# Performance work log

Hardware: AMD Instinct MI355X
Metric: run time of the kernel (lower is better)

The kernel has to match this reference:

```python
import jax, jax.numpy as jnp
import numpy as np

N_HITS = 16384
N_EDGES = 262144
N_GROUPS = 512
N_EVENTS = 64
IN_CH = 25
HID = 128
HEADS = 4
DH = HID // HEADS
LAYERS = 3
EDGE_DIM = 5
FFN = 4 * HID
EPS = 1e-5


def setup_inputs() -> dict:
    key = jax.random.key(0)
    ks = jax.random.split(key, 16)
    def nrm(k, shape, s=0.05):
        return jax.random.normal(k, shape, dtype=jnp.float32) * s
    z = lambda *s: jnp.zeros(s, jnp.float32)
    return {
        "x": jax.random.normal(ks[0], (N_HITS, IN_CH), dtype=jnp.float32),
        "edge_index": jax.random.randint(ks[1], (2, N_EDGES), 0, N_HITS, dtype=jnp.int32),
        "edge_attr": jax.random.normal(ks[2], (N_EDGES, EDGE_DIM), dtype=jnp.float32),
        "group_indices": jax.random.randint(ks[3], (N_HITS,), 0, N_GROUPS, dtype=jnp.int32),
        "batch_indices_per_group": jnp.sort(jax.random.randint(ks[4], (N_GROUPS,), 0, N_EVENTS, dtype=jnp.int32)),
        "embed_W": nrm(ks[5], (IN_CH, HID)),
        "embed_b": z(HID),
        "blk_Wqkv": nrm(ks[6], (LAYERS, HID, 3 * HID)),
        "blk_bqkv": z(LAYERS, 3 * HID),
        "blk_We": nrm(ks[7], (LAYERS, EDGE_DIM, HID)),
        "blk_be": z(LAYERS, HID),
        "blk_Wo": nrm(ks[8], (LAYERS, HID, HID)),
        "blk_bo": z(LAYERS, HID),
        "ln1_g": jnp.ones((LAYERS, HID), jnp.float32),
        "ln1_b": z(LAYERS, HID),
        "ffn_W1": nrm(ks[9], (LAYERS, HID, FFN)),
        "ffn_b1": z(LAYERS, FFN),
        "ffn_W2": nrm(ks[10], (LAYERS, FFN, HID)),
        "ffn_b2": z(LAYERS, HID),
        "ln2_g": jnp.ones((LAYERS, HID), jnp.float32),
        "ln2_b": z(LAYERS, HID),
        "aff_W1": nrm(ks[11], (4 * HID, HID)),
        "aff_b1": z(HID),
        "aff_W2": nrm(ks[12], (HID, 1)),
        "aff_b2": z(1),
    }


def _layer_norm(v, g, b):
    mu = jnp.mean(v, axis=-1, keepdims=True)
    var = jnp.mean((v - mu) ** 2, axis=-1, keepdims=True)
    return (v - mu) * jax.lax.rsqrt(var + EPS) * g + b


def reference(x, edge_index, edge_attr, group_indices, batch_indices_per_group,
              embed_W, embed_b, blk_Wqkv, blk_bqkv, blk_We, blk_be, blk_Wo, blk_bo,
              ln1_g, ln1_b, ffn_W1, ffn_b1, ffn_W2, ffn_b2, ln2_g, ln2_b,
              aff_W1, aff_b1, aff_W2, aff_b2):
    n = x.shape[0]
    G = batch_indices_per_group.shape[0]
    src, dst = edge_index[0], edge_index[1]
    scale = 1.0 / np.sqrt(DH).astype(np.float32)

    h = x @ embed_W + embed_b  # [N, HID]
    for l in range(LAYERS):
        # edge-conditioned multi-head attention over the graph edges
        qkv = h @ blk_Wqkv[l] + blk_bqkv[l]
        q, k, v = jnp.split(qkv, 3, axis=-1)
        e = edge_attr @ blk_We[l] + blk_be[l]          # [E, HID]
        qe = q[dst].reshape(-1, HEADS, DH)              # [E, h, d]
        ke = (k[src] + e).reshape(-1, HEADS, DH)
        ve = (v[src] + e).reshape(-1, HEADS, DH)
        logits = jnp.einsum("ehd,ehd->eh", qe, ke) * scale
        m = jax.ops.segment_max(logits, dst, num_segments=n)
        m = jnp.where(jnp.isfinite(m), m, 0.0)          # nodes with no in-edges
        p = jnp.exp(logits - m[dst])
        s = jax.ops.segment_sum(p, dst, num_segments=n)
        attn = jax.ops.segment_sum(p[:, :, None] * ve, dst, num_segments=n)
        attn = (attn / jnp.maximum(s, 1e-9)[:, :, None]).reshape(n, HID)
        h = _layer_norm(h + attn @ blk_Wo[l] + blk_bo[l], ln1_g[l], ln1_b[l])
        f = jax.nn.relu(h @ ffn_W1[l] + ffn_b1[l]) @ ffn_W2[l] + ffn_b2[l]
        h = _layer_norm(h + f, ln2_g[l], ln2_b[l])

    # group pooling (multi-scatter)
    raw_view = x[:, 3].astype(jnp.int32)  # truncation, matches torch .long()
    cnt_all = jax.ops.segment_sum(jnp.ones((n,), jnp.float32), group_indices, num_segments=G)
    g_max = jax.ops.segment_max(h, group_indices, num_segments=G)
    g_max = jnp.where(cnt_all[:, None] > 0, g_max, 0.0)  # torch_scatter fills empty with 0

    def pool_view(view_id):
        w = (raw_view == view_id).astype(jnp.float32)
        cnt = jax.ops.segment_sum(w, group_indices, num_segments=G)
        summ = jax.ops.segment_sum(h * w[:, None], group_indices, num_segments=G)
        pooled = summ / jnp.maximum(cnt, 1.0)[:, None]
        has = (cnt > 0).astype(jnp.float32)[:, None]
        return pooled, has

    pool_x, has_x = pool_view(0)
    pool_y, has_y = pool_view(1)
    sum_feat = pool_x * has_x + pool_y * has_y
    valid = jnp.maximum(has_x + has_y, 1.0)
    ge = jnp.concatenate([sum_feat / valid, g_max], axis=1)  # [G, 2*HID]

    # pairwise affinity MLP: Linear(4H->H) split so the [G,G,4H] concat is never built
    W1a, W1b = aff_W1[: 2 * HID], aff_W1[2 * HID:]
    pre = (ge @ W1a)[:, None, :] + (ge @ W1b)[None, :, :] + aff_b1  # [G, G, HID]
    scores = (jax.nn.relu(pre) @ aff_W2 + aff_b2)[..., 0]           # [G, G]
    scores = 0.5 * (scores + scores.T)
    event_mask = batch_indices_per_group[:, None] == batch_indices_per_group[None, :]
    return jax.nn.sigmoid(scores) * event_mask.astype(scores.dtype)
```

## Files before the change

### kernel.cpp

```cpp
#include <hip/hip_runtime.h>
#include <hip/hip_bf16.h>

#define NHITS   16384
#define NEDGES  262144
#define NGROUPS 512
#define HID     128
#define LAYERS  3
#define FFND    512
#define MAXDEG  64
#define GCAP    96

typedef __attribute__((ext_vector_type(8))) short bf16x8;
typedef __attribute__((ext_vector_type(8))) unsigned short ushort8;
typedef __attribute__((ext_vector_type(4))) float floatx4;

__device__ __forceinline__ float bf2f(ushort u) {
    return __uint_as_float(((unsigned)u) << 16);
}
__device__ __forceinline__ ushort f2bf(float f) {
    unsigned u = __float_as_uint(f);
    unsigned r = (u + 0x7FFFu + ((u >> 16) & 1u)) >> 16;
    return (ushort)r;
}

__device__ __forceinline__ void gl2lds16(const ushort* gp, ushort* lp) {
    __builtin_amdgcn_global_load_lds(
        (const __attribute__((address_space(1))) unsigned int*)(gp),
        (__attribute__((address_space(3))) unsigned int*)(lp), 16, 0, 0);
}


struct TD { const float* src; ushort* dst; int K; int N; };
struct TDs { TD d[14]; };

__global__ __launch_bounds__(256) void transpose_all(TDs tds, int* __restrict__ zbuf,
                                                     int ztotal) {
    __shared__ float lds[32][33];
    if (blockIdx.y == 0) {
        for (int gz = blockIdx.x * 256 + threadIdx.x; gz < ztotal; gz += 64 * 256)
            zbuf[gz] = 0;
    }
    TD d = tds.d[blockIdx.y];
    int tX = d.N >> 5;
    int tiles = (d.K >> 5) * tX;
    if ((int)blockIdx.x >= tiles) return;
    int tk = blockIdx.x / tX, tn = blockIdx.x % tX;
    int k0 = tk * 32, n0 = tn * 32;
    int r = threadIdx.x >> 5, c = threadIdx.x & 31;
#pragma unroll
    for (int i = 0; i < 4; ++i)
        lds[r + i * 8][c] = d.src[(size_t)(k0 + r + i * 8) * d.N + n0 + c];
    __syncthreads();
#pragma unroll
    for (int i = 0; i < 4; ++i) {
        int n = n0 + r + i * 8;
        d.dst[(size_t)n * d.K + k0 + c] = f2bf(lds[c][r + i * 8]);
    }
}


__global__ __launch_bounds__(256) void scatter_embed(
        const int* __restrict__ src, const int* __restrict__ dst,
        const float* __restrict__ ea, const int* __restrict__ gidx,
        int* __restrict__ cnt, int* __restrict__ cnt2,
        int4* __restrict__ epk, int* __restrict__ hlist,
        const float* __restrict__ x, const float* __restrict__ embW,
        const float* __restrict__ embB, float* __restrict__ h,
        ushort* __restrict__ hb) {
    const int vb = blockIdx.x, t = threadIdx.x;
    if (vb < 1024) {
        int e = vb * 256 + t;
        int d = dst[e];
        int slot = atomicAdd(&cnt[d], 1);
        if (slot < MAXDEG) {
            const float* eap = ea + (size_t)e * 5;
            int4 m;
            m.x = src[e];
            m.y = (int)((unsigned)f2bf(eap[0]) | ((unsigned)f2bf(eap[1]) << 16));
            m.z = (int)((unsigned)f2bf(eap[2]) | ((unsigned)f2bf(eap[3]) << 16));
            m.w = (int)(unsigned)f2bf(eap[4]);
            epk[(size_t)d * MAXDEG + slot] = m;
        }
        if (e < NHITS) {
            int g = gidx[e];
            int slot2 = atomicAdd(&cnt2[g], 1);
            if (slot2 < GCAP) hlist[g * GCAP + slot2] = e;
        }
    } else {
        __shared__ float xs[2][32];
        int base = (vb - 1024) * 32;
        for (int it = 0; it < 16; ++it) {
            int i0 = base + it * 2;
            __syncthreads();
            if (t < 25) xs[0][t] = x[(size_t)i0 * 25 + t];
            else if (t >= 128 && t < 153) xs[1][t - 128] = x[(size_t)(i0 + 1) * 25 + (t - 128)];
            __syncthreads();
            int node = i0 + (t >> 7), c = t & 127;
            const float* xr = xs[t >> 7];
            float s = embB[c];
#pragma unroll
            for (int k = 0; k < 25; ++k) s += xr[k] * embW[k * HID + c];
            h[(size_t)node * HID + c] = s;
            hb[(size_t)node * HID + c] = f2bf(s);
        }
    }
}


__global__ __launch_bounds__(256) void gemm_mfma_k(const ushort* __restrict__ A,
                                                   const ushort* __restrict__ Bt,
                                                   const float* __restrict__ bias,
                                                   ushort* __restrict__ C,
                                                   int N, int K, int relu) {
    __shared__ ushort As[128 * 32];
    __shared__ ushort Bs[128 * 32];
    const int t = threadIdx.x;
    const int lane = t & 63;
    const int w = t >> 6;
    const int wr = w >> 1, wc = w & 1;
    const int lm = lane & 15, q = lane >> 4;
    const int row0 = blockIdx.y * 128;
    const int col0 = blockIdx.x * 128;
    const int sr = t >> 2, sc = (t & 3) * 8;
    const int sr2 = (t + 256) >> 2, sc2 = ((t + 256) & 3) * 8;

    floatx4 acc[4][4] = {};
    for (int k0 = 0; k0 < K; k0 += 32) {
        gl2lds16(A + (size_t)(row0 + sr) * K + k0 + sc,   &As[t * 8]);
        gl2lds16(A + (size_t)(row0 + sr2) * K + k0 + sc2, &As[t * 8 + 2048]);
        gl2lds16(Bt + (size_t)(col0 + sr) * K + k0 + sc,   &Bs[t * 8]);
        gl2lds16(Bt + (size_t)(col0 + sr2) * K + k0 + sc2, &Bs[t * 8 + 2048]);
        __syncthreads();
        bf16x8 af[4], bf[4];
#pragma unroll
        for (int it = 0; it < 4; ++it)
            af[it] = *(const bf16x8*)&As[(wr * 64 + it * 16 + lm) * 32 + q * 8];
#pragma unroll
        for (int jt = 0; jt < 4; ++jt)
            bf[jt] = *(const bf16x8*)&Bs[(wc * 64 + jt * 16 + lm) * 32 + q * 8];
#pragma unroll
        for (int it = 0; it < 4; ++it)
#pragma unroll
            for (int jt = 0; jt < 4; ++jt)
                acc[it][jt] = __builtin_amdgcn_mfma_f32_16x16x32_bf16(
                    af[it], bf[jt], acc[it][jt], 0, 0, 0);
        __syncthreads();
    }
#pragma unroll
    for (int jt = 0; jt < 4; ++jt) {
        int col = col0 + wc * 64 + jt * 16 + lm;
        float bb = bias ? bias[col] : 0.f;
#pragma unroll
        for (int it = 0; it < 4; ++it)
#pragma unroll
            for (int r = 0; r < 4; ++r) {
                int row = row0 + wr * 64 + it * 16 + q * 4 + r;
                float o = acc[it][jt][r] + bb;
                if (relu) o = fmaxf(o, 0.f);
                C[(size_t)row * N + col] = f2bf(o);
            }
    }
}


__global__ __launch_bounds__(256) void gemm_qkv_k(const ushort* __restrict__ A,
                                                  const ushort* __restrict__ Bt,
                                                  const float* __restrict__ bias,
                                                  ushort* __restrict__ qb,
                                                  ushort* __restrict__ kvb,
                                                  int K) {
    __shared__ ushort As[128 * 32];
    __shared__ ushort Bs[128 * 32];
    const int t = threadIdx.x;
    const int lane = t & 63;
    const int w = t >> 6;
    const int wr = w >> 1, wc = w & 1;
    const int lm = lane & 15, q = lane >> 4;
    const int row0 = blockIdx.y * 128;
    const int col0 = blockIdx.x * 128;
    const int sr = t >> 2, sc = (t & 3) * 8;
    const int sr2 = (t + 256) >> 2, sc2 = ((t + 256) & 3) * 8;

    floatx4 acc[4][4] = {};
    for (int k0 = 0; k0 < K; k0 += 32) {
        gl2lds16(A + (size_t)(row0 + sr) * K + k0 + sc,   &As[t * 8]);
        gl2lds16(A + (size_t)(row0 + sr2) * K + k0 + sc2, &As[t * 8 + 2048]);
        gl2lds16(Bt + (size_t)(col0 + sr) * K + k0 + sc,   &Bs[t * 8]);
        gl2lds16(Bt + (size_t)(col0 + sr2) * K + k0 + sc2, &Bs[t * 8 + 2048]);
        __syncthreads();
        bf16x8 af[4], bf[4];
#pragma unroll
        for (int it = 0; it < 4; ++it)
            af[it] = *(const bf16x8*)&As[(wr * 64 + it * 16 + lm) * 32 + q * 8];
#pragma unroll
        for (int jt = 0; jt < 4; ++jt)
            bf[jt] = *(const bf16x8*)&Bs[(wc * 64 + jt * 16 + lm) * 32 + q * 8];
#pragma unroll
        for (int it = 0; it < 4; ++it)
#pragma unroll
            for (int jt = 0; jt < 4; ++jt)
                acc[it][jt] = __builtin_amdgcn_mfma_f32_16x16x32_bf16(
                    af[it], bf[jt], acc[it][jt], 0, 0, 0);
        __syncthreads();
    }
#pragma unroll
    for (int jt = 0; jt < 4; ++jt) {
        int col = col0 + wc * 64 + jt * 16 + lm;
        float bb = bias[col];
#pragma unroll
        for (int it = 0; it < 4; ++it)
#pragma unroll
            for (int r = 0; r < 4; ++r) {
                int row = row0 + wr * 64 + it * 16 + q * 4 + r;
                ushort ob = f2bf(acc[it][jt][r] + bb);
                if (col < 128) qb[(size_t)row * 128 + col] = ob;
                else           kvb[(size_t)row * 256 + (col - 128)] = ob;
            }
    }
}


__global__ __launch_bounds__(256) void attn_kernel(const ushort* __restrict__ qb,
                                                   const ushort* __restrict__ kvb,
                                                   const int4* __restrict__ epk,
                                                   const int* __restrict__ cnt,
                                                   const float* __restrict__ We,
                                                   const float* __restrict__ be,
                                                   ushort* __restrict__ attnb) {
    __shared__ float WeS[640], beS[128];
    int t = threadIdx.x;
    for (int idx = t; idx < 640; idx += 256) WeS[idx] = We[idx];
    if (t < 128) beS[t] = be[t];
    __syncthreads();
    const int i = blockIdx.x * 4 + (t >> 6);
    const int lane = t & 63;
    const int grp = lane >> 4;
    const int cb = (lane & 15) * 8;
    float qv[8];
    {
        ushort8 qq = *(const ushort8*)(qb + (size_t)i * 128 + cb);
#pragma unroll
        for (int j = 0; j < 8; ++j) qv[j] = bf2f(qq[j]);
    }
    float pj[6];
#pragma unroll
    for (int k = 0; k < 5; ++k) {
        float s = 0.f;
#pragma unroll
        for (int j = 0; j < 8; ++j) s += qv[j] * WeS[k * 128 + cb + j];
        pj[k] = s;
    }
    {
        float sb = 0.f;
#pragma unroll
        for (int j = 0; j < 8; ++j) sb += qv[j] * beS[cb + j];
        pj[5] = sb;
    }
#pragma unroll
    for (int k = 0; k < 6; ++k) {
        pj[k] += __shfl_xor(pj[k], 1);
        pj[k] += __shfl_xor(pj[k], 2);
    }
    float S = 0.f, T0 = 0.f, T1 = 0.f, T2 = 0.f, T3 = 0.f, T4 = 0.f;
    float acc[8] = {};
    const int endc = min(cnt[i], MAXDEG);
    const size_t pbase = (size_t)i * MAXDEG;
    const float scale = 0.17677669529663687f;

#pragma unroll 4
    for (int p0 = 0; p0 < endc; p0 += 4) {
        int pp = p0 + grp;
        bool act = pp < endc;
        int slot = act ? pp : (endc - 1);
        int4 m = epk[pbase + slot];
        int s = m.x;
        float a0 = bf2f((ushort)((unsigned)m.y & 0xffffu));
        float a1 = bf2f((ushort)((unsigned)m.y >> 16));
        float a2 = bf2f((ushort)((unsigned)m.z & 0xffffu));
        float a3 = bf2f((ushort)((unsigned)m.z >> 16));
        float a4 = bf2f((ushort)((unsigned)m.w & 0xffffu));
        const ushort* srow = kvb + (size_t)s * 256;
        ushort8 kk = *(const ushort8*)(srow + cb);
        ushort8 vv = *(const ushort8*)(srow + 128 + cb);
        float part = 0.f;
#pragma unroll
        for (int j = 0; j < 8; ++j) part += qv[j] * bf2f(kk[j]);
        part += __shfl_xor(part, 1);
        part += __shfl_xor(part, 2);
        float logit = (part + pj[5] + a0 * pj[0] + a1 * pj[1] + a2 * pj[2]
                       + a3 * pj[3] + a4 * pj[4]) * scale;
        float pe = act ? __expf(logit) : 0.f;
        S += pe;
        T0 += pe * a0; T1 += pe * a1; T2 += pe * a2; T3 += pe * a3; T4 += pe * a4;
#pragma unroll
        for (int j = 0; j < 8; ++j) acc[j] += pe * bf2f(vv[j]);
    }
#pragma unroll
    for (int j = 0; j < 8; ++j) {
        acc[j] += __shfl_xor(acc[j], 16);
        acc[j] += __shfl_xor(acc[j], 32);
    }
    S += __shfl_xor(S, 16);   S += __shfl_xor(S, 32);
    T0 += __shfl_xor(T0, 16); T0 += __shfl_xor(T0, 32);
    T1 += __shfl_xor(T1, 16); T1 += __shfl_xor(T1, 32);
    T2 += __shfl_xor(T2, 16); T2 += __shfl_xor(T2, 32);
    T3 += __shfl_xor(T3, 16); T3 += __shfl_xor(T3, 32);
    T4 += __shfl_xor(T4, 16); T4 += __shfl_xor(T4, 32);
    if (grp == 0) {
        float inv = 1.f / fmaxf(S, 1e-9f);
        ushort8 o;
#pragma unroll
        for (int j = 0; j < 8; ++j) {
            float wadd = WeS[cb + j] * T0 + WeS[128 + cb + j] * T1
                       + WeS[256 + cb + j] * T2 + WeS[384 + cb + j] * T3
                       + WeS[512 + cb + j] * T4 + beS[cb + j] * S;
            o[j] = f2bf((acc[j] + wadd) * inv);
        }
        *(ushort8*)(attnb + (size_t)i * HID + cb) = o;
    }
}


__global__ __launch_bounds__(256) void woffn_k(
        const ushort* __restrict__ attnb,
        const ushort* __restrict__ Wot, const float* __restrict__ bo,
        const float* __restrict__ ln1g, const float* __restrict__ ln1b,
        const ushort* __restrict__ W1t, const float* __restrict__ b1v,
        const ushort* __restrict__ W2t, const float* __restrict__ b2v,
        const float* __restrict__ ln2g, const float* __restrict__ ln2b,
        float* __restrict__ h,
        const ushort* __restrict__ Wqn, const float* __restrict__ bqn,
        ushort* __restrict__ qb, ushort* __restrict__ kvb) {
    __shared__ ushort As[32 * 136];
    __shared__ ushort Bs[4 * 4096];
    __shared__ ushort midc[32 * 136];
    __shared__ float redS[64], redQ[64];
    const int t = threadIdx.x;
    const int lane = t & 63;
    const int w = t >> 6;
    const int wr = w >> 1, wc = w & 1;
    const int lm = lane & 15, q = lane >> 4;
    const int row0 = blockIdx.x * 32;
    const int sr = t >> 2, sc = (t & 3) * 8;
    const int sr2 = (t + 256) >> 2, sc2 = ((t + 256) & 3) * 8;

    auto stageB = [&](const ushort* Wt, int ldK, int koff) {
#pragma unroll
        for (int kc = 0; kc < 4; ++kc) {
            gl2lds16(Wt + (size_t)sr * ldK + koff + kc * 32 + sc,
                     &Bs[kc * 4096 + t * 8]);
            gl2lds16(Wt + (size_t)sr2 * ldK + koff + kc * 32 + sc2,
                     &Bs[kc * 4096 + t * 8 + 2048]);
        }
    };
    auto gemmK = [&](const ushort* Alds, floatx4* acc) {
#pragma unroll
        for (int kc = 0; kc < 4; ++kc) {
            bf16x8 af = *(const bf16x8*)&Alds[(wr * 16 + lm) * 136 + kc * 32 + q * 8];
#pragma unroll
            for (int jt = 0; jt < 4; ++jt) {
                bf16x8 bf = *(const bf16x8*)&Bs[kc * 4096 + (wc * 64 + jt * 16 + lm) * 32 + q * 8];
                acc[jt] = __builtin_amdgcn_mfma_f32_16x16x32_bf16(af, bf, acc[jt], 0, 0, 0);
            }
        }
    };

    for (int i = t; i < 32 * 16; i += 256) {
        int row = i >> 4, c8 = (i & 15) * 8;
        *(ushort8*)&As[row * 136 + c8] =
            *(const ushort8*)(attnb + (size_t)(row0 + row) * HID + c8);
    }
    stageB(Wot, HID, 0);
    __syncthreads();

    floatx4 accW[4] = {};
    gemmK(As, accW);

    float o1[4][4];
    {
        float psum[4] = {}, psq[4] = {};
#pragma unroll
        for (int jt = 0; jt < 4; ++jt) {
            int col = wc * 64 + jt * 16 + lm;
            float bb = bo[col];
#pragma unroll
            for (int r = 0; r < 4; ++r) {
                int row = row0 + wr * 16 + q * 4 + r;
                float v = accW[jt][r] + bb + h[(size_t)row * HID + col];
                o1[jt][r] = v;
                psum[r] += v;
                psq[r] += v * v;
            }
        }
#pragma unroll
        for (int r = 0; r < 4; ++r) {
            float s = psum[r], ss = psq[r];
#pragma unroll
            for (int k = 1; k < 16; k <<= 1) {
                s += __shfl_xor(s, k, 16);
                ss += __shfl_xor(ss, k, 16);
            }
            psum[r] = s; psq[r] = ss;
        }
        if (lm == 0)
#pragma unroll
            for (int r = 0; r < 4; ++r) {
                int rl = wr * 16 + q * 4 + r;
                redS[rl * 2 + wc] = psum[r];
                redQ[rl * 2 + wc] = psq[r];
            }
        __syncthreads();
#pragma unroll
        for (int r = 0; r < 4; ++r) {
            int rl = wr * 16 + q * 4 + r;
            float tot = redS[rl * 2] + redS[rl * 2 + 1];
            float totq = redQ[rl * 2] + redQ[rl * 2 + 1];
            float mu = tot * (1.f / HID);
            float var = totq * (1.f / HID) - mu * mu;
            float rstd = rsqrtf(var + 1e-5f);
#pragma unroll
            for (int jt = 0; jt < 4; ++jt) {
                int col = wc * 64 + jt * 16 + lm;
                float o = (o1[jt][r] - mu) * rstd * ln1g[col] + ln1b[col];
                o1[jt][r] = o;
                As[(wr * 16 + q * 4 + r) * 136 + col] = f2bf(o);
            }
        }
    }

    floatx4 acc2[4] = {};
    for (int nc = 0; nc < 4; ++nc) {
        __syncthreads();
        stageB(W1t + (size_t)nc * 128 * HID, HID, 0);
        __syncthreads();
        floatx4 acc1[4] = {};
        gemmK(As, acc1);
#pragma unroll
        for (int jt = 0; jt < 4; ++jt) {
            int col = wc * 64 + jt * 16 + lm;
            float bb = b1v[nc * 128 + col];
#pragma unroll
            for (int r = 0; r < 4; ++r) {
                int row = wr * 16 + q * 4 + r;
                midc[row * 136 + col] = f2bf(fmaxf(acc1[jt][r] + bb, 0.f));
            }
        }
        __syncthreads();
        stageB(W2t, FFND, nc * 128);
        __syncthreads();
        gemmK(midc, acc2);
    }

    {
        float psum[4] = {}, psq[4] = {};
#pragma unroll
        for (int jt = 0; jt < 4; ++jt) {
            int col = wc * 64 + jt * 16 + lm;
            float bb = b2v[col];
#pragma unroll
            for (int r = 0; r < 4; ++r) {
                float v = acc2[jt][r] + bb + o1[jt][r];
                acc2[jt][r] = v;
                psum[r] += v;
                psq[r] += v * v;
            }
        }
#pragma unroll
        for (int r = 0; r < 4; ++r) {
            float s = psum[r], ss = psq[r];
#pragma unroll
            for (int k = 1; k < 16; k <<= 1) {
                s += __shfl_xor(s, k, 16);
                ss += __shfl_xor(ss, k, 16);
            }
            psum[r] = s; psq[r] = ss;
        }
        if (lm == 0)
#pragma unroll
            for (int r = 0; r < 4; ++r) {
                int rl = wr * 16 + q * 4 + r;
                redS[rl * 2 + wc] = psum[r];
                redQ[rl * 2 + wc] = psq[r];
            }
        __syncthreads();
#pragma unroll
        for (int r = 0; r < 4; ++r) {
            int rl = wr * 16 + q * 4 + r;
            float tot = redS[rl * 2] + redS[rl * 2 + 1];
            float totq = redQ[rl * 2] + redQ[rl * 2 + 1];
            float mu = tot * (1.f / HID);
            float var = totq * (1.f / HID) - mu * mu;
            float rstd = rsqrtf(var + 1e-5f);
            int row = row0 + rl;
#pragma unroll
            for (int jt = 0; jt < 4; ++jt) {
                int col = wc * 64 + jt * 16 + lm;
                float o = (acc2[jt][r] - mu) * rstd * ln2g[col] + ln2b[col];
                h[(size_t)row * HID + col] = o;
                if (Wqn) As[rl * 136 + col] = f2bf(o);
            }
        }
    }
    if (!Wqn) return;

    for (int nc = 0; nc < 3; ++nc) {
        __syncthreads();
        stageB(Wqn + (size_t)nc * 128 * HID, HID, 0);
        __syncthreads();
        floatx4 accq[4] = {};
        gemmK(As, accq);
#pragma unroll
        for (int jt = 0; jt < 4; ++jt) {
            int col = wc * 64 + jt * 16 + lm;
            float bb = bqn[nc * 128 + col];
#pragma unroll
            for (int r = 0; r < 4; ++r) {
                int row = row0 + wr * 16 + q * 4 + r;
                ushort ob = f2bf(accq[jt][r] + bb);
                if (nc == 0)      qb[(size_t)row * 128 + col] = ob;
                else if (nc == 1) kvb[(size_t)row * 256 + col] = ob;
                else              kvb[(size_t)row * 256 + 128 + col] = ob;
            }
        }
    }
}


__global__ __launch_bounds__(128) void pool_group(const float* __restrict__ h,
                                                  const float* __restrict__ x,
                                                  const int* __restrict__ hlist,
                                                  const int* __restrict__ cnt2,
                                                  ushort* __restrict__ geb) {
    int g = blockIdx.x, c = threadIdx.x;
    int n = min(cnt2[g], GCAP);
    float mx = -INFINITY, sx = 0.f, sy = 0.f, cx = 0.f, cy = 0.f;
    for (int p = 0; p < n; ++p) {
        int i = hlist[g * GCAP + p];
        float hv = h[(size_t)i * HID + c];
        mx = fmaxf(mx, hv);
        int view = (int)x[(size_t)i * 25 + 3];
        if (view == 0) { sx += hv; cx += 1.f; }
        else if (view == 1) { sy += hv; cy += 1.f; }
    }
    float gm = (n > 0) ? mx : 0.f;
    float px = sx / fmaxf(cx, 1.f), py = sy / fmaxf(cy, 1.f);
    float hx = cx > 0.f ? 1.f : 0.f, hy = cy > 0.f ? 1.f : 0.f;
    float sf = px * hx + py * hy;
    float valid = fmaxf(hx + hy, 1.f);
    geb[g * 256 + c] = f2bf(sf / valid);
    geb[g * 256 + 128 + c] = f2bf(gm);
}


__global__ __launch_bounds__(256) void score_final(const ushort* __restrict__ Cab,
                                                   const float* __restrict__ W2,
                                                   const float* __restrict__ b1v,
                                                   const float* __restrict__ b2,
                                                   const int* __restrict__ ev,
                                                   float* __restrict__ out) {
    int bi = blockIdx.y, bj = blockIdx.x;
    if (bj < bi) return;
    __shared__ float Ai[16][129], Bi[16][129], Aj[16][129], Bj[16][129];
    __shared__ float w2s[128], b1s[128];
    int t = threadIdx.y * 16 + threadIdx.x;
    int i0 = bi * 16, j0 = bj * 16;
    for (int idx = t; idx < 2048; idx += 256) {
        int r = idx >> 7, k = idx & 127;
        Ai[r][k] = bf2f(Cab[(size_t)(i0 + r) * 256 + k]);
        Bi[r][k] = bf2f(Cab[(size_t)(i0 + r) * 256 + 128 + k]);
        Aj[r][k] = bf2f(Cab[(size_t)(j0 + r) * 256 + k]);
        Bj[r][k] = bf2f(Cab[(size_t)(j0 + r) * 256 + 128 + k]);
    }
    if (t < 128) { w2s[t] = W2[t]; b1s[t] = b1v[t]; }
    __syncthreads();
    int tx = threadIdx.x, ty = threadIdx.y;
    float sij = 0.f, sji = 0.f;
#pragma unroll 4
    for (int k = 0; k < 128; ++k) {
        float pb = b1s[k], wk = w2s[k];
        sij += fmaxf(Ai[ty][k] + Bj[tx][k] + pb, 0.f) * wk;
        sji += fmaxf(Aj[tx][k] + Bi[ty][k] + pb, 0.f) * wk;
    }
    float z = 0.5f * (sij + sji) + b2[0];
    float sg = 1.f / (1.f + __expf(-z));
    int gi = i0 + ty, gj = j0 + tx;
    float res = (ev[gi] == ev[gj]) ? sg : 0.f;
    out[(size_t)gi * NGROUPS + gj] = res;
    out[(size_t)gj * NGROUPS + gi] = res;
}


static inline char* align256(char* p) {
    return (char*)(((uintptr_t)p + 255) & ~(uintptr_t)255);
}

extern "C" void kernel_launch(void* const* d_in, const int* in_sizes, int n_in,
                              void* d_out, int out_size, void* d_ws, size_t ws_size,
                              hipStream_t stream) {
    const float* x    = (const float*)d_in[0];
    const int* eidx   = (const int*)d_in[1];
    const float* ea   = (const float*)d_in[2];
    const int* gidx   = (const int*)d_in[3];
    const int* ev     = (const int*)d_in[4];
    const float* embW = (const float*)d_in[5];
    const float* embB = (const float*)d_in[6];
    const float* Wqkv = (const float*)d_in[7];
    const float* bqkv = (const float*)d_in[8];
    const float* We   = (const float*)d_in[9];
    const float* be   = (const float*)d_in[10];
    const float* Wo   = (const float*)d_in[11];
    const float* bo   = (const float*)d_in[12];
    const float* ln1g = (const float*)d_in[13];
    const float* ln1b = (const float*)d_in[14];
    const float* W1   = (const float*)d_in[15];
    const float* b1   = (const float*)d_in[16];
    const float* W2   = (const float*)d_in[17];
    const float* b2   = (const float*)d_in[18];
    const float* ln2g = (const float*)d_in[19];
    const float* ln2b = (const float*)d_in[20];
    const float* affW1 = (const float*)d_in[21];
    const float* affb1 = (const float*)d_in[22];
    const float* affW2 = (const float*)d_in[23];
    const float* affb2 = (const float*)d_in[24];

    const int* src = eidx;
    const int* dst = eidx + NEDGES;

    char* p = (char*)d_ws;
    float* h    = (float*)p;            p += (size_t)NHITS * HID * 4;
    int* cnt    = (int*)p;              p += NHITS * 4;
    int* cnt2   = (int*)p;              p += NGROUPS * 4;
    int* hlist  = (int*)p;              p += NGROUPS * GCAP * 4;
    p = align256(p);
    int4* epk   = (int4*)p;             p += (size_t)NHITS * MAXDEG * 16;
    ushort* hb    = (ushort*)p;         p += (size_t)NHITS * HID * 2;
    ushort* qb    = (ushort*)p;         p += (size_t)NHITS * 128 * 2;
    ushort* kvb   = (ushort*)p;         p += (size_t)NHITS * 256 * 2;
    ushort* attnb = (ushort*)p;         p += (size_t)NHITS * HID * 2;
    ushort* geb   = (ushort*)p;         p += (size_t)NGROUPS * 256 * 2;
    ushort* Cab   = (ushort*)p;         p += (size_t)NGROUPS * 256 * 2;
    p = align256(p);
    ushort* Wqkvt = (ushort*)p;         p += (size_t)LAYERS * 384 * HID * 2;
    ushort* Wot   = (ushort*)p;         p += (size_t)LAYERS * HID * HID * 2;
    ushort* W1t   = (ushort*)p;         p += (size_t)LAYERS * FFND * HID * 2;
    ushort* W2t   = (ushort*)p;         p += (size_t)LAYERS * HID * FFND * 2;
    ushort* W1abt = (ushort*)p;         p += (size_t)256 * 256 * 2;

    TDs tds;
    for (int l = 0; l < LAYERS; ++l) {
        tds.d[l * 4 + 0] = { Wqkv + (size_t)l * HID * 384, Wqkvt + (size_t)l * 384 * HID, HID, 384 };
        tds.d[l * 4 + 1] = { Wo + (size_t)l * HID * HID,   Wot + (size_t)l * HID * HID,   HID, HID };
        tds.d[l * 4 + 2] = { W1 + (size_t)l * HID * FFND,  W1t + (size_t)l * FFND * HID,  HID, FFND };
        tds.d[l * 4 + 3] = { W2 + (size_t)l * FFND * HID,  W2t + (size_t)l * HID * FFND,  FFND, HID };
    }
    tds.d[12] = { affW1,             W1abt,             256, HID };
    tds.d[13] = { affW1 + 256 * HID, W1abt + 128 * 256, 256, HID };
    transpose_all<<<dim3(64, 14), 256, 0, stream>>>(tds, cnt, NHITS + NGROUPS);

    scatter_embed<<<1536, 256, 0, stream>>>(src, dst, ea, gidx, cnt, cnt2,
                                            epk, hlist, x, embW, embB, h, hb);

    gemm_qkv_k<<<dim3(3, NHITS / 128), 256, 0, stream>>>(
        hb, Wqkvt, bqkv, qb, kvb, HID);

    for (int l = 0; l < LAYERS; ++l) {
        attn_kernel<<<NHITS / 4, 256, 0, stream>>>(
            qb, kvb, epk, cnt, We + (size_t)l * 5 * HID, be + l * HID, attnb);
        const ushort* Wqn = (l + 1 < LAYERS) ? Wqkvt + (size_t)(l + 1) * 384 * HID : nullptr;
        const float* bqn = (l + 1 < LAYERS) ? bqkv + (l + 1) * 384 : nullptr;
        woffn_k<<<NHITS / 32, 256, 0, stream>>>(
            attnb, Wot + (size_t)l * HID * HID, bo + l * HID,
            ln1g + l * HID, ln1b + l * HID,
            W1t + (size_t)l * FFND * HID, b1 + l * FFND,
            W2t + (size_t)l * HID * FFND, b2 + l * HID,
            ln2g + l * HID, ln2b + l * HID, h, Wqn, bqn, qb, kvb);
    }

    pool_group<<<NGROUPS, 128, 0, stream>>>(h, x, hlist, cnt2, geb);
    gemm_mfma_k<<<dim3(2, NGROUPS / 128), 256, 0, stream>>>(
        geb, W1abt, nullptr, Cab, 256, 256, 0);
    score_final<<<dim3(NGROUPS / 16, NGROUPS / 16), dim3(16, 16), 0, stream>>>(
        Cab, affW2, affb1, affb2, ev, (float*)d_out);
}
```

Measured before the change: 347.1 us.

## Prefetch next weight tile into registers while current MFMA GEMM runs

Replaces the synchronous global-to-LDS weight staging in the fused Wo/LN/FFN/LN/QKV kernel with a register double-buffer. The next B tile is loaded into registers before each GEMM and written to shared memory afterwards, so global weight latency overlaps with MFMA work instead of stalling between stages. The cost is 32 extra VGPRs per thread, which may lower occupancy. It also issues a dummy prefetch of Wot on the last layer, where no QKV projection follows.

```diff
diff --git a/kernel.cpp b/kernel.cpp
--- a/kernel.cpp
+++ b/kernel.cpp
@@ -344,13 +344,19 @@
     const int sr = t >> 2, sc = (t & 3) * 8;
     const int sr2 = (t + 256) >> 2, sc2 = ((t + 256) & 3) * 8;
 
-    auto stageB = [&](const ushort* Wt, int ldK, int koff) {
+    ushort8 pf[8];
+    auto pref = [&](const ushort* Wt, int ldK, int koff) {
 #pragma unroll
         for (int kc = 0; kc < 4; ++kc) {
-            gl2lds16(Wt + (size_t)sr * ldK + koff + kc * 32 + sc,
-                     &Bs[kc * 4096 + t * 8]);
-            gl2lds16(Wt + (size_t)sr2 * ldK + koff + kc * 32 + sc2,
-                     &Bs[kc * 4096 + t * 8 + 2048]);
+            pf[kc * 2]     = *(const ushort8*)(Wt + (size_t)sr * ldK + koff + kc * 32 + sc);
+            pf[kc * 2 + 1] = *(const ushort8*)(Wt + (size_t)sr2 * ldK + koff + kc * 32 + sc2);
+        }
+    };
+    auto commit = [&]() {
+#pragma unroll
+        for (int kc = 0; kc < 4; ++kc) {
+            *(ushort8*)&Bs[kc * 4096 + t * 8] = pf[kc * 2];
+            *(ushort8*)&Bs[kc * 4096 + t * 8 + 2048] = pf[kc * 2 + 1];
         }
     };
     auto gemmK = [&](const ushort* Alds, floatx4* acc) {
@@ -370,9 +376,12 @@
         *(ushort8*)&As[row * 136 + c8] =
             *(const ushort8*)(attnb + (size_t)(row0 + row) * HID + c8);
     }
-    stageB(Wot, HID, 0);
+    pref(Wot, HID, 0);
     __syncthreads();
-
+    commit();
+    __syncthreads();
+
+    pref(W1t, HID, 0);
     floatx4 accW[4] = {};
     gemmK(As, accW);
 
@@ -427,12 +436,13 @@
             }
         }
     }
+    __syncthreads();
+    commit();
+    __syncthreads();
 
     floatx4 acc2[4] = {};
     for (int nc = 0; nc < 4; ++nc) {
-        __syncthreads();
-        stageB(W1t + (size_t)nc * 128 * HID, HID, 0);
-        __syncthreads();
+        pref(W2t, FFND, nc * 128);
         floatx4 acc1[4] = {};
         gemmK(As, acc1);
 #pragma unroll
@@ -446,9 +456,14 @@
             }
         }
         __syncthreads();
-        stageB(W2t, FFND, nc * 128);
-        __syncthreads();
+        commit();
+        __syncthreads();
+        if (nc < 3) pref(W1t + (size_t)(nc + 1) * 128 * HID, HID, 0);
+        else        pref(Wqn ? Wqn : Wot, HID, 0);
         gemmK(midc, acc2);
+        __syncthreads();
+        commit();
+        __syncthreads();
     }
 
     {
@@ -502,11 +517,10 @@
         }
     }
     if (!Wqn) return;
+    __syncthreads();
 
     for (int nc = 0; nc < 3; ++nc) {
-        __syncthreads();
-        stageB(Wqn + (size_t)nc * 128 * HID, HID, 0);
-        __syncthreads();
+        if (nc < 2) pref(Wqn + (size_t)(nc + 1) * 128 * HID, HID, 0);
         floatx4 accq[4] = {};
         gemmK(As, accq);
 #pragma unroll
@@ -521,6 +535,11 @@
                 else if (nc == 1) kvb[(size_t)row * 256 + col] = ob;
                 else              kvb[(size_t)row * 256 + 128 + col] = ob;
             }
+        }
+        if (nc < 2) {
+            __syncthreads();
+            commit();
+            __syncthreads();
         }
     }
 }
```

After: 347.1 us. Within noise of the previous version (+0.0%).

## Fuse embedding with layer-0 QKV GEMM and pooling with affinity projection

Applied to the files above, without the earlier changes.

The embedding blocks now keep their 32 embedded rows in shared memory as bf16 and run the layer-0 QKV projection with MFMA right there. This removes the hb buffer round trip and the separate QKV GEMM launch. Group pooling is likewise fused with the 256x256 affinity projection as a plain FMA dot product in the same kernel, which drops the geb buffer and the MFMA GEMM launch. In exchange, each embed block reloads the full QKV weight, shared memory per block grows to about 41 KB, and the scatter blocks also reserve that shared memory.

```diff
diff --git a/kernel.cpp b/kernel.cpp
--- a/kernel.cpp
+++ b/kernel.cpp
@@ -59,14 +59,16 @@
 }
 
 
-__global__ __launch_bounds__(256) void scatter_embed(
+__global__ __launch_bounds__(256) void scatter_embed_qkv(
         const int* __restrict__ src, const int* __restrict__ dst,
         const float* __restrict__ ea, const int* __restrict__ gidx,
         int* __restrict__ cnt, int* __restrict__ cnt2,
         int4* __restrict__ epk, int* __restrict__ hlist,
         const float* __restrict__ x, const float* __restrict__ embW,
         const float* __restrict__ embB, float* __restrict__ h,
-        ushort* __restrict__ hb) {
+        const ushort* __restrict__ Wq0, const float* __restrict__ bq0,
+        ushort* __restrict__ qb, ushort* __restrict__ kvb) {
+    __shared__ __align__(16) char smem[8704 + 4 * 8192];
     const int vb = blockIdx.x, t = threadIdx.x;
     if (vb < 1024) {
         int e = vb * 256 + t;
@@ -86,136 +88,67 @@
             int slot2 = atomicAdd(&cnt2[g], 1);
             if (slot2 < GCAP) hlist[g * GCAP + slot2] = e;
         }
-    } else {
-        __shared__ float xs[2][32];
-        int base = (vb - 1024) * 32;
-        for (int it = 0; it < 16; ++it) {
-            int i0 = base + it * 2;
-            __syncthreads();
-            if (t < 25) xs[0][t] = x[(size_t)i0 * 25 + t];
-            else if (t >= 128 && t < 153) xs[1][t - 128] = x[(size_t)(i0 + 1) * 25 + (t - 128)];
-            __syncthreads();
-            int node = i0 + (t >> 7), c = t & 127;
-            const float* xr = xs[t >> 7];
-            float s = embB[c];
-#pragma unroll
-            for (int k = 0; k < 25; ++k) s += xr[k] * embW[k * HID + c];
-            h[(size_t)node * HID + c] = s;
-            hb[(size_t)node * HID + c] = f2bf(s);
-        }
-    }
-}
-
-
-__global__ __launch_bounds__(256) void gemm_mfma_k(const ushort* __restrict__ A,
-                                                   const ushort* __restrict__ Bt,
-                                                   const float* __restrict__ bias,
-                                                   ushort* __restrict__ C,
-                                                   int N, int K, int relu) {
-    __shared__ ushort As[128 * 32];
-    __shared__ ushort Bs[128 * 32];
-    const int t = threadIdx.x;
+        return;
+    }
+    ushort* As = (ushort*)smem;
+    ushort* Bs = (ushort*)(smem + 8704);
+    float* xsF = (float*)(smem + 8704);
+    const int base = (vb - 1024) * 32;
+
+    for (int i = t; i < 32 * 25; i += 256) {
+        int node = i / 25, k = i - node * 25;
+        xsF[node * 26 + k] = x[(size_t)(base + node) * 25 + k];
+    }
+    __syncthreads();
+    for (int i = t; i < 32 * 128; i += 256) {
+        int node = i >> 7, c = i & 127;
+        float s = embB[c];
+#pragma unroll
+        for (int k = 0; k < 25; ++k) s += xsF[node * 26 + k] * embW[k * HID + c];
+        h[(size_t)(base + node) * HID + c] = s;
+        As[node * 136 + c] = f2bf(s);
+    }
+
     const int lane = t & 63;
     const int w = t >> 6;
     const int wr = w >> 1, wc = w & 1;
     const int lm = lane & 15, q = lane >> 4;
-    const int row0 = blockIdx.y * 128;
-    const int col0 = blockIdx.x * 128;
     const int sr = t >> 2, sc = (t & 3) * 8;
     const int sr2 = (t + 256) >> 2, sc2 = ((t + 256) & 3) * 8;
 
-    floatx4 acc[4][4] = {};
-    for (int k0 = 0; k0 < K; k0 += 32) {
-        gl2lds16(A + (size_t)(row0 + sr) * K + k0 + sc,   &As[t * 8]);
-        gl2lds16(A + (size_t)(row0 + sr2) * K + k0 + sc2, &As[t * 8 + 2048]);
-        gl2lds16(Bt + (size_t)(col0 + sr) * K + k0 + sc,   &Bs[t * 8]);
-        gl2lds16(Bt + (size_t)(col0 + sr2) * K + k0 + sc2, &Bs[t * 8 + 2048]);
-        __syncthreads();
-        bf16x8 af[4], bf[4];
-#pragma unroll
-        for (int it = 0; it < 4; ++it)
-            af[it] = *(const bf16x8*)&As[(wr * 64 + it * 16 + lm) * 32 + q * 8];
-#pragma unroll
-        for (int jt = 0; jt < 4; ++jt)
-            bf[jt] = *(const bf16x8*)&Bs[(wc * 64 + jt * 16 + lm) * 32 + q * 8];
-#pragma unroll
-        for (int it = 0; it < 4; ++it)
-#pragma unroll
-            for (int jt = 0; jt < 4; ++jt)
-                acc[it][jt] = __builtin_amdgcn_mfma_f32_16x16x32_bf16(
-                    af[it], bf[jt], acc[it][jt], 0, 0, 0);
-        __syncthreads();
-    }
-#pragma unroll
-    for (int jt = 0; jt < 4; ++jt) {
-        int col = col0 + wc * 64 + jt * 16 + lm;
-        float bb = bias ? bias[col] : 0.f;
-#pragma unroll
-        for (int it = 0; it < 4; ++it)
+    for (int nc = 0; nc < 3; ++nc) {
+        __syncthreads();
+#pragma unroll
+        for (int kc = 0; kc < 4; ++kc) {
+            gl2lds16(Wq0 + (size_t)(nc * 128 + sr) * HID + kc * 32 + sc,
+                     &Bs[kc * 4096 + t * 8]);
+            gl2lds16(Wq0 + (size_t)(nc * 128 + sr2) * HID + kc * 32 + sc2,
+                     &Bs[kc * 4096 + t * 8 + 2048]);
+        }
+        __syncthreads();
+        floatx4 accq[4] = {};
+#pragma unroll
+        for (int kc = 0; kc < 4; ++kc) {
+            bf16x8 af = *(const bf16x8*)&As[(wr * 16 + lm) * 136 + kc * 32 + q * 8];
+#pragma unroll
+            for (int jt = 0; jt < 4; ++jt) {
+                bf16x8 bf = *(const bf16x8*)&Bs[kc * 4096 + (wc * 64 + jt * 16 + lm) * 32 + q * 8];
+                accq[jt] = __builtin_amdgcn_mfma_f32_16x16x32_bf16(af, bf, accq[jt], 0, 0, 0);
+            }
+        }
+#pragma unroll
+        for (int jt = 0; jt < 4; ++jt) {
+            int col = wc * 64 + jt * 16 + lm;
+            float bb = bq0[nc * 128 + col];
 #pragma unroll
             for (int r = 0; r < 4; ++r) {
-                int row = row0 + wr * 64 + it * 16 + q * 4 + r;
-                float o = acc[it][jt][r] + bb;
-                if (relu) o = fmaxf(o, 0.f);
-                C[(size_t)row * N + col] = f2bf(o);
-            }
-    }
-}
-
-
-__global__ __launch_bounds__(256) void gemm_qkv_k(const ushort* __restrict__ A,
-                                                  const ushort* __restrict__ Bt,
-                                                  const float* __restrict__ bias,
-                                                  ushort* __restrict__ qb,
-                                                  ushort* __restrict__ kvb,
-                                                  int K) {
-    __shared__ ushort As[128 * 32];
-    __shared__ ushort Bs[128 * 32];
-    const int t = threadIdx.x;
-    const int lane = t & 63;
-    const int w = t >> 6;
-    const int wr = w >> 1, wc = w & 1;
-    const int lm = lane & 15, q = lane >> 4;
-    const int row0 = blockIdx.y * 128;
-    const int col0 = blockIdx.x * 128;
-    const int sr = t >> 2, sc = (t & 3) * 8;
-    const int sr2 = (t + 256) >> 2, sc2 = ((t + 256) & 3) * 8;
-
-    floatx4 acc[4][4] = {};
-    for (int k0 = 0; k0 < K; k0 += 32) {
-        gl2lds16(A + (size_t)(row0 + sr) * K + k0 + sc,   &As[t * 8]);
-        gl2lds16(A + (size_t)(row0 + sr2) * K + k0 + sc2, &As[t * 8 + 2048]);
-        gl2lds16(Bt + (size_t)(col0 + sr) * K + k0 + sc,   &Bs[t * 8]);
-        gl2lds16(Bt + (size_t)(col0 + sr2) * K + k0 + sc2, &Bs[t * 8 + 2048]);
-        __syncthreads();
-        bf16x8 af[4], bf[4];
-#pragma unroll
-        for (int it = 0; it < 4; ++it)
-            af[it] = *(const bf16x8*)&As[(wr * 64 + it * 16 + lm) * 32 + q * 8];
-#pragma unroll
-        for (int jt = 0; jt < 4; ++jt)
-            bf[jt] = *(const bf16x8*)&Bs[(wc * 64 + jt * 16 + lm) * 32 + q * 8];
-#pragma unroll
-        for (int it = 0; it < 4; ++it)
-#pragma unroll
-            for (int jt = 0; jt < 4; ++jt)
-                acc[it][jt] = __builtin_amdgcn_mfma_f32_16x16x32_bf16(
-                    af[it], bf[jt], acc[it][jt], 0, 0, 0);
-        __syncthreads();
-    }
-#pragma unroll
-    for (int jt = 0; jt < 4; ++jt) {
-        int col = col0 + wc * 64 + jt * 16 + lm;
-        float bb = bias[col];
-#pragma unroll
-        for (int it = 0; it < 4; ++it)
-#pragma unroll
-            for (int r = 0; r < 4; ++r) {
-                int row = row0 + wr * 64 + it * 16 + q * 4 + r;
-                ushort ob = f2bf(acc[it][jt][r] + bb);
-                if (col < 128) qb[(size_t)row * 128 + col] = ob;
-                else           kvb[(size_t)row * 256 + (col - 128)] = ob;
-            }
+                int row = base + wr * 16 + q * 4 + r;
+                ushort ob = f2bf(accq[jt][r] + bb);
+                if (nc == 0)      qb[(size_t)row * 128 + col] = ob;
+                else if (nc == 1) kvb[(size_t)row * 256 + col] = ob;
+                else              kvb[(size_t)row * 256 + 128 + col] = ob;
+            }
+        }
     }
 }
 
@@ -526,29 +459,51 @@
 }
 
 
-__global__ __launch_bounds__(128) void pool_group(const float* __restrict__ h,
+__global__ __launch_bounds__(256) void pool_aff_k(const float* __restrict__ h,
                                                   const float* __restrict__ x,
                                                   const int* __restrict__ hlist,
                                                   const int* __restrict__ cnt2,
-                                                  ushort* __restrict__ geb) {
-    int g = blockIdx.x, c = threadIdx.x;
-    int n = min(cnt2[g], GCAP);
-    float mx = -INFINITY, sx = 0.f, sy = 0.f, cx = 0.f, cy = 0.f;
-    for (int p = 0; p < n; ++p) {
-        int i = hlist[g * GCAP + p];
-        float hv = h[(size_t)i * HID + c];
-        mx = fmaxf(mx, hv);
-        int view = (int)x[(size_t)i * 25 + 3];
-        if (view == 0) { sx += hv; cx += 1.f; }
-        else if (view == 1) { sy += hv; cy += 1.f; }
-    }
-    float gm = (n > 0) ? mx : 0.f;
-    float px = sx / fmaxf(cx, 1.f), py = sy / fmaxf(cy, 1.f);
-    float hx = cx > 0.f ? 1.f : 0.f, hy = cy > 0.f ? 1.f : 0.f;
-    float sf = px * hx + py * hy;
-    float valid = fmaxf(hx + hy, 1.f);
-    geb[g * 256 + c] = f2bf(sf / valid);
-    geb[g * 256 + 128 + c] = f2bf(gm);
+                                                  const ushort* __restrict__ W1abt,
+                                                  ushort* __restrict__ Cab) {
+    __shared__ float gebS[2][256];
+    const int t = threadIdx.x;
+    const int g0 = blockIdx.x * 2;
+    {
+        int gg = t >> 7, c = t & 127;
+        int g = g0 + gg;
+        int n = min(cnt2[g], GCAP);
+        float mx = -INFINITY, sx = 0.f, sy = 0.f, cx = 0.f, cy = 0.f;
+        for (int p = 0; p < n; ++p) {
+            int i = hlist[g * GCAP + p];
+            float hv = h[(size_t)i * HID + c];
+            mx = fmaxf(mx, hv);
+            int view = (int)x[(size_t)i * 25 + 3];
+            if (view == 0) { sx += hv; cx += 1.f; }
+            else if (view == 1) { sy += hv; cy += 1.f; }
+        }
+        float gm = (n > 0) ? mx : 0.f;
+        float px = sx / fmaxf(cx, 1.f), py = sy / fmaxf(cy, 1.f);
+        float hx = cx > 0.f ? 1.f : 0.f, hy = cy > 0.f ? 1.f : 0.f;
+        float sf = px * hx + py * hy;
+        float valid = fmaxf(hx + hy, 1.f);
+        gebS[gg][c] = sf / valid;
+        gebS[gg][128 + c] = gm;
+    }
+    __syncthreads();
+    float a0 = 0.f, a1 = 0.f;
+    const ushort8* wrow = (const ushort8*)(W1abt + (size_t)t * 256);
+#pragma unroll 8
+    for (int kk = 0; kk < 32; ++kk) {
+        ushort8 wv = wrow[kk];
+#pragma unroll
+        for (int j = 0; j < 8; ++j) {
+            float wf = bf2f(wv[j]);
+            a0 += gebS[0][kk * 8 + j] * wf;
+            a1 += gebS[1][kk * 8 + j] * wf;
+        }
+    }
+    Cab[(size_t)g0 * 256 + t] = f2bf(a0);
+    Cab[(size_t)(g0 + 1) * 256 + t] = f2bf(a1);
 }
 
 
@@ -633,11 +588,9 @@
     int* hlist  = (int*)p;              p += NGROUPS * GCAP * 4;
     p = align256(p);
     int4* epk   = (int4*)p;             p += (size_t)NHITS * MAXDEG * 16;
-    ushort* hb    = (ushort*)p;         p += (size_t)NHITS * HID * 2;
     ushort* qb    = (ushort*)p;         p += (size_t)NHITS * 128 * 2;
     ushort* kvb   = (ushort*)p;         p += (size_t)NHITS * 256 * 2;
     ushort* attnb = (ushort*)p;         p += (size_t)NHITS * HID * 2;
-    ushort* geb   = (ushort*)p;         p += (size_t)NGROUPS * 256 * 2;
     ushort* Cab   = (ushort*)p;         p += (size_t)NGROUPS * 256 * 2;
     p = align256(p);
     ushort* Wqkvt = (ushort*)p;         p += (size_t)LAYERS * 384 * HID * 2;
@@ -657,11 +610,9 @@
     tds.d[13] = { affW1 + 256 * HID, W1abt + 128 * 256, 256, HID };
     transpose_all<<<dim3(64, 14), 256, 0, stream>>>(tds, cnt, NHITS + NGROUPS);
 
-    scatter_embed<<<1536, 256, 0, stream>>>(src, dst, ea, gidx, cnt, cnt2,
-                                            epk, hlist, x, embW, embB, h, hb);
-
-    gemm_qkv_k<<<dim3(3, NHITS / 128), 256, 0, stream>>>(
-        hb, Wqkvt, bqkv, qb, kvb, HID);
+    scatter_embed_qkv<<<1536, 256, 0, stream>>>(src, dst, ea, gidx, cnt, cnt2,
+                                                epk, hlist, x, embW, embB, h,
+                                                Wqkvt, bqkv, qb, kvb);
 
     for (int l = 0; l < LAYERS; ++l) {
         attn_kernel<<<NHITS / 4, 256, 0, stream>>>(
@@ -676,9 +627,7 @@
             ln2g + l * HID, ln2b + l * HID, h, Wqn, bqn, qb, kvb);
     }
 
-    pool_group<<<NGROUPS, 128, 0, stream>>>(h, x, hlist, cnt2, geb);
-    gemm_mfma_k<<<dim3(2, NGROUPS / 128), 256, 0, stream>>>(
-        geb, W1abt, nullptr, Cab, 256, 256, 0);
+    pool_aff_k<<<NGROUPS / 2, 256, 0, stream>>>(h, x, hlist, cnt2, W1abt, Cab);
     score_final<<<dim3(NGROUPS / 16, NGROUPS / 16), dim3(16, 16), 0, stream>>>(
         Cab, affW2, affb1, affb2, ev, (float*)d_out);
 }
```

New measurement: 344.4 us. About the same (-0.8%).
